# Optimization experiments

Measured on AMD Instinct MI355X. Metric: run time of the kernel, lower is better.

## Reference

```python
import jax, jax.numpy as jnp
import numpy as np

B, N, DIM = 4, 1024, 768
H, D = 12, 64            # num_heads, head_dim
R = 8                    # spd_rank
INNER = H * D
SCALE = D ** -0.5


def setup_inputs() -> dict:
    key = jax.random.key(0)
    ks = jax.random.split(key, 8)
    def w(k, shp, s=0.02):
        return jax.random.normal(k, shp, jnp.float32) * s
    return {
        "x": jax.random.normal(ks[0], (B, N, DIM), jnp.float32),
        # VariationalLinear params: weight mean mu + log-sigma (for KL term)
        "wq_mu": w(ks[1], (INNER, DIM)), "wq_ls": jnp.full((INNER, DIM), -5.0, jnp.float32),
        "wk_mu": w(ks[2], (INNER, DIM)), "wk_ls": jnp.full((INNER, DIM), -5.0, jnp.float32),
        "wv_mu": w(ks[3], (INNER, DIM)), "wv_ls": jnp.full((INNER, DIM), -5.0, jnp.float32),
        "wo_mu": w(ks[4], (DIM, INNER)), "wo_ls": jnp.full((DIM, INNER), -5.0, jnp.float32),
        "wo_b": jnp.zeros((DIM,), jnp.float32),
        # LogEuclideanProjection linear layers (head_dim -> spd_rank)
        "sq_w": w(ks[5], (R, D)), "sq_b": jnp.zeros((R,), jnp.float32),
        "sk_w": w(ks[6], (R, D)), "sk_b": jnp.zeros((R,), jnp.float32),
    }


def _kl(mu, ls):
    # KL( N(mu, sigma^2) || N(0,1) ) summed over weights
    return 0.5 * jnp.sum(jnp.exp(2.0 * ls) + mu * mu - 1.0 - 2.0 * ls)


def reference(x, wq_mu, wq_ls, wk_mu, wk_ls, wv_mu, wv_ls,
              wo_mu, wo_ls, wo_b, sq_w, sq_b, sk_w, sk_b):
    b, n, _ = x.shape
    # Q/K/V projections (variational linear, mean weights)
    q = jnp.einsum('bnd,id->bni', x, wq_mu).reshape(b, n, H, D).transpose(0, 2, 1, 3)
    k = jnp.einsum('bnd,id->bni', x, wk_mu).reshape(b, n, H, D).transpose(0, 2, 1, 3)
    v = jnp.einsum('bnd,id->bni', x, wv_mu).reshape(b, n, H, D).transpose(0, 2, 1, 3)

    # SPD projection (diagonal SPD): softplus(linear) + 1e-6, per head token
    q_spd = jax.nn.softplus(jnp.einsum('bhnd,rd->bhnr', q, sq_w) + sq_b) + 1e-6
    k_spd = jax.nn.softplus(jnp.einsum('bhnd,rd->bhnr', k, sk_w) + sk_b) + 1e-6
    lq = jnp.log(q_spd + 1e-8)  # (b,h,n,R)
    lk = jnp.log(k_spd + 1e-8)

    # ||lq_i - lk_j||_2 via expansion (avoids (b,h,n,n,R) intermediate)
    d2 = (jnp.sum(lq * lq, -1)[..., :, None]
          + jnp.sum(lk * lk, -1)[..., None, :]
          - 2.0 * jnp.einsum('bhnr,bhmr->bhnm', lq, lk))
    dist = jnp.sqrt(jnp.maximum(d2, 1e-12))  # (b,h,n,n)

    attn = jax.nn.softmax(-dist * SCALE, axis=-1)
    out = jnp.einsum('bhnm,bhmd->bhnd', attn, v)
    out = out.transpose(0, 2, 1, 3).reshape(b, n, INNER)
    out = jnp.einsum('bni,di->bnd', out, wo_mu) + wo_b

    kl_total = _kl(wq_mu, wq_ls) + _kl(wk_mu, wk_ls) + _kl(wv_mu, wv_ls) + _kl(wo_mu, wo_ls)
    return out, kl_total
```

## Files before the change

kernel.cpp:

```cpp
#include <hip/hip_runtime.h>
#include <math.h>

#define HQ   12
#define DH   64
#define NSEQ 1024
#define BB   4
#define DIMM 768
#define RR   8
#define BHD  (BB*HQ)
#define MROWS (BB*NSEQ)
#define OUT_ELEMS (BB*NSEQ*DIMM)

typedef short bf16x8 __attribute__((ext_vector_type(8)));
typedef float f32x4  __attribute__((ext_vector_type(4)));

__device__ __forceinline__ unsigned short f2bf(float f) {
    union { float f; unsigned u; } x; x.f = f;
    return (unsigned short)((x.u + 0x7fffu + ((x.u >> 16) & 1u)) >> 16);
}
__device__ __forceinline__ float bf2f(unsigned short b) {
    union { unsigned u; float f; } x; x.u = ((unsigned)b) << 16;
    return x.f;
}
__device__ __forceinline__ unsigned pack_bf16(float w0, float w1) {
    return __builtin_amdgcn_perm(__float_as_uint(w1) + 0x8000u,
                                 __float_as_uint(w0) + 0x8000u, 0x07060302u);
}

#define AS_GLOBAL(p) ((const __attribute__((address_space(1))) void*)(p))
#define AS_LDS(p)    ((__attribute__((address_space(3))) void*)(p))

__global__ __launch_bounds__(256)
void prep_kernel(const float* __restrict__ x,  const float* __restrict__ wv,
                 const float* __restrict__ wo, const float* __restrict__ wq,
                 const float* __restrict__ wq_ls, const float* __restrict__ wk,
                 const float* __restrict__ wk_ls, const float* __restrict__ wv_ls,
                 const float* __restrict__ wo_ls, const float* __restrict__ sqw,
                 const float* __restrict__ skw,
                 unsigned short* __restrict__ xb, unsigned short* __restrict__ wvb,
                 unsigned short* __restrict__ wob, unsigned short* __restrict__ cqk,
                 double* __restrict__ klacc)
{
    __shared__ double sd[256];
    const int seg = blockIdx.y;
    const int tid = threadIdx.x;
    const int bx  = blockIdx.x;

    if (seg <= 2) {
        const float* src = (seg == 0) ? x : (seg == 1) ? wv : wo;
        unsigned short* dst = (seg == 0) ? xb : (seg == 1) ? wvb : wob;
        const int n4 = (seg == 0) ? 786432 : 147456;
        for (int i = bx*256 + tid; i < n4; i += 1024*256) {
            float4 v = ((const float4*)src)[i];
            ((uint2*)dst)[i] = make_uint2(pack_bf16(v.x, v.y), pack_bf16(v.z, v.w));
        }
    } else if (seg <= 6) {
        if (bx >= 64) return;
        const float *mu, *ls;
        if      (seg == 3) { mu = wq; ls = wq_ls; }
        else if (seg == 4) { mu = wk; ls = wk_ls; }
        else if (seg == 5) { mu = wv; ls = wv_ls; }
        else               { mu = wo; ls = wo_ls; }
        double acc = 0.0;
        for (int i = bx*256 + tid; i < 147456; i += 64*256) {
            float4 m4 = ((const float4*)mu)[i];
            float4 l4 = ((const float4*)ls)[i];
            acc += (double)(expf(2.f*l4.x) + m4.x*m4.x - 1.f - 2.f*l4.x);
            acc += (double)(expf(2.f*l4.y) + m4.y*m4.y - 1.f - 2.f*l4.y);
            acc += (double)(expf(2.f*l4.z) + m4.z*m4.z - 1.f - 2.f*l4.z);
            acc += (double)(expf(2.f*l4.w) + m4.w*m4.w - 1.f - 2.f*l4.w);
        }
        sd[tid] = acc;
        __syncthreads();
        for (int s = 128; s > 0; s >>= 1) {
            if (tid < s) sd[tid] += sd[tid + s];
            __syncthreads();
        }
        if (tid == 0) atomicAdd(klacc, sd[0]);
    } else {
        if (bx >= 576) return;
        const int j   = (bx % 3)*256 + tid;
        const int row = bx / 3;
        const int g   = row >= 96;
        const int hr  = row - g*96;
        const int h   = hr >> 3, r = hr & 7;
        const float* sw = (g ? skw : sqw) + r*64;
        const float* W  = (g ? wk  : wq) + h*64*768 + j;
        float acc = 0.f;
        #pragma unroll
        for (int d = 0; d < 64; ++d) acc += sw[d] * W[d*768];
        cqk[row*768 + j] = f2bf(acc);
    }
}

__global__ __launch_bounds__(256)
void lspd_gemm(const unsigned short* __restrict__ X,
               const unsigned short* __restrict__ Cqk,
               const float* __restrict__ sqb, const float* __restrict__ skb,
               unsigned short* __restrict__ lqo, unsigned short* __restrict__ lko,
               float* __restrict__ nqo, float* __restrict__ nko)
{
    __shared__ unsigned short As[64*32];
    __shared__ unsigned short Bs[64*32];
    const int tid  = threadIdx.x;
    const int lane = tid & 63;
    const int qr   = lane & 15, quad = lane >> 4;
    const int wid  = tid >> 6;
    const int w_m  = wid >> 1, w_n = wid & 1;
    const int bx = blockIdx.x, by = blockIdx.y;
    const int row0 = tid >> 2;
    const int segk = (tid & 3) * 8;

    f32x4 acc[2][2] = {};

    for (int kt = 0; kt < 768; kt += 32) {
        __syncthreads();
        __builtin_amdgcn_global_load_lds(AS_GLOBAL(X   + (by*64 + row0)*768 + kt + segk),
                                         AS_LDS(&As[tid*8]), 16, 0, 0);
        __builtin_amdgcn_global_load_lds(AS_GLOBAL(Cqk + (bx*64 + row0)*768 + kt + segk),
                                         AS_LDS(&Bs[tid*8]), 16, 0, 0);
        __syncthreads();

        bf16x8 a[2], b[2];
        #pragma unroll
        for (int mi = 0; mi < 2; ++mi)
            a[mi] = *(const bf16x8*)&As[(w_m*32 + mi*16 + qr)*32 + quad*8];
        #pragma unroll
        for (int ni = 0; ni < 2; ++ni)
            b[ni] = *(const bf16x8*)&Bs[(w_n*32 + ni*16 + qr)*32 + quad*8];
        #pragma unroll
        for (int mi = 0; mi < 2; ++mi)
            #pragma unroll
            for (int ni = 0; ni < 2; ++ni)
                acc[mi][ni] = __builtin_amdgcn_mfma_f32_16x16x32_bf16(a[mi], b[ni], acc[mi][ni], 0, 0, 0);
    }

    const int rr = qr & 7;
    #pragma unroll
    for (int ni = 0; ni < 2; ++ni) {
        const int c = bx*64 + w_n*32 + ni*16 + qr;
        const int g = (c >= 96);
        const int cc = c - g*96;
        const int h = cc >> 3;
        unsigned short* dst = g ? lko : lqo;
        float* ndst = g ? nko : nqo;
        const float bias = (g ? skb : sqb)[rr];
        #pragma unroll
        for (int mi = 0; mi < 2; ++mi) {
            #pragma unroll
            for (int r = 0; r < 4; ++r) {
                const int m = by*64 + w_m*32 + mi*16 + quad*4 + r;
                const int b = m >> 10, n = m & 1023;
                const float pre = acc[mi][ni][r] + bias;
                const float sp = (pre > 0.f) ? (pre + log1pf(__expf(-pre)))
                                             : log1pf(__expf(pre));
                const float l = __logf(sp + 1e-6f + 1e-8f);
                const unsigned short lb = f2bf(l);
                const int base = ((b*HQ + h) << 10) + n;
                dst[(base << 3) + rr] = lb;
                const float lr = bf2f(lb);
                float sq = lr * lr;
                sq += __shfl_xor(sq, 1);
                sq += __shfl_xor(sq, 2);
                sq += __shfl_xor(sq, 4);
                if (rr == 0) ndst[base] = sq;
            }
        }
    }
}

template<int MODE>
__global__ __launch_bounds__(256)
void mfma_gemm(const unsigned short* __restrict__ X,
               const unsigned short* __restrict__ Wf,
               const float* __restrict__ bias,
               unsigned short* __restrict__ vt, float* __restrict__ outp,
               const double* __restrict__ klacc)
{
    __shared__ unsigned short As[64*32];
    __shared__ unsigned short Bs[64*32];
    const int tid  = threadIdx.x;
    const int lane = tid & 63;
    const int qr   = lane & 15, quad = lane >> 4;
    const int wid  = tid >> 6;
    const int w_m  = wid >> 1, w_n = wid & 1;
    const int bx = blockIdx.x, by = blockIdx.y;

    const unsigned short* Abase = (MODE == 0) ? (Wf + bx*64*768) : (X + by*64*768);
    const unsigned short* Bbase = (MODE == 0) ? (X + by*64*768) : (Wf + bx*64*768);

    const int row0 = tid >> 2;
    const int segk = (tid & 3) * 8;

    f32x4 acc[2][2] = {};

    for (int kt = 0; kt < 768; kt += 32) {
        __syncthreads();
        __builtin_amdgcn_global_load_lds(AS_GLOBAL(Abase + row0*768 + kt + segk),
                                         AS_LDS(&As[tid*8]), 16, 0, 0);
        __builtin_amdgcn_global_load_lds(AS_GLOBAL(Bbase + row0*768 + kt + segk),
                                         AS_LDS(&Bs[tid*8]), 16, 0, 0);
        __syncthreads();

        bf16x8 a[2], b[2];
        #pragma unroll
        for (int mi = 0; mi < 2; ++mi)
            a[mi] = *(const bf16x8*)&As[(w_m*32 + mi*16 + qr)*32 + quad*8];
        #pragma unroll
        for (int ni = 0; ni < 2; ++ni)
            b[ni] = *(const bf16x8*)&Bs[(w_n*32 + ni*16 + qr)*32 + quad*8];
        #pragma unroll
        for (int mi = 0; mi < 2; ++mi)
            #pragma unroll
            for (int ni = 0; ni < 2; ++ni)
                acc[mi][ni] = __builtin_amdgcn_mfma_f32_16x16x32_bf16(a[mi], b[ni], acc[mi][ni], 0, 0, 0);
    }

    if (MODE == 1) {
        #pragma unroll
        for (int ni = 0; ni < 2; ++ni) {
            const int i = bx*64 + w_n*32 + ni*16 + qr;
            const float bs = bias[i];
            #pragma unroll
            for (int mi = 0; mi < 2; ++mi) {
                const int m0 = by*64 + w_m*32 + mi*16 + quad*4;
                #pragma unroll
                for (int r = 0; r < 4; ++r)
                    outp[(m0 + r)*768 + i] = acc[mi][ni][r] + bs;
            }
        }
        if (bx == 0 && by == 0 && tid == 0)
            outp[OUT_ELEMS] = (float)(0.5 * klacc[0]);
    } else {
        const int bidx = (by*64) >> 10;
        #pragma unroll
        for (int mi = 0; mi < 2; ++mi) {
            #pragma unroll
            for (int r = 0; r < 4; ++r) {
                const int i = bx*64 + w_m*32 + mi*16 + quad*4 + r;
                const int h = i >> 6, d = i & 63;
                #pragma unroll
                for (int ni = 0; ni < 2; ++ni) {
                    const int n = by*64 + w_n*32 + ni*16 + qr;
                    vt[((((bidx*HQ + h) << 6) + d) << 10) + (n & 1023)] = f2bf(acc[mi][ni][r]);
                }
            }
        }
    }
}

__global__ __launch_bounds__(256)
void attn_kernel(const unsigned short* __restrict__ lq,
                 const unsigned short* __restrict__ lk,
                 const float* __restrict__ nq, const float* __restrict__ nk,
                 const unsigned short* __restrict__ vt,
                 unsigned short* __restrict__ out)
{
    __shared__ unsigned short lk_s[64*8];
    __shared__ unsigned short vt_s[64*64];
    __shared__ unsigned short w_s[64*72];

    const int tid  = threadIdx.x;
    const int lane = tid & 63;
    const int wid  = tid >> 6;
    const int qr   = lane & 15;
    const int quad = lane >> 4;
    const int bh   = blockIdx.y;
    const int q0   = blockIdx.x*64 + wid*16;
    const int qrow = (bh << 10) + q0 + qr;
    const int bb   = bh / HQ;
    const int hh   = bh - bb*HQ;

    bf16x8 bq = {};
    if (quad == 0) bq = *(const bf16x8*)(lq + qrow*8);
    const float nqv = nq[qrow];

    f32x4 acc[4] = {};
    float wsum_acc = 0.f;

    const unsigned short* vtg = vt + (bh << 16);
    const unsigned short* lkg = lk + (bh << 13);
    const float*          nkg = nk + (bh << 10);

    const int srow = tid >> 3;
    const int scol = ((tid & 7) ^ (srow & 7)) << 3;
    const float EXP2S = -0.1803368801f;

    for (int c = 0; c < NSEQ; c += 64) {
        __syncthreads();
        __builtin_amdgcn_global_load_lds(AS_GLOBAL(vtg + srow*1024 + c + scol),
                                         AS_LDS(&vt_s[tid*8]), 16, 0, 0);
        __builtin_amdgcn_global_load_lds(AS_GLOBAL(vtg + (srow + 32)*1024 + c + scol),
                                         AS_LDS(&vt_s[2048 + tid*8]), 16, 0, 0);
        if (tid < 64)
            __builtin_amdgcn_global_load_lds(AS_GLOBAL(lkg + (c + tid)*8),
                                             AS_LDS(&lk_s[tid*8]), 16, 0, 0);
        __syncthreads();

        float wsum_c = 0.f;
        unsigned wpk[4][2];
        #pragma unroll
        for (int kb = 0; kb < 4; ++kb) {
            bf16x8 ak = {};
            if (quad == 0) ak = *(const bf16x8*)&lk_s[(kb*16 + qr)*8];
            f32x4 s = {};
            s = __builtin_amdgcn_mfma_f32_16x16x32_bf16(ak, bq, s, 0, 0, 0);
            const float4 nk4 = *(const float4*)(nkg + c + kb*16 + quad*4);
            const float nkv[4] = {nk4.x, nk4.y, nk4.z, nk4.w};
            float w[4];
            #pragma unroll
            for (int r = 0; r < 4; ++r) {
                const float d2 = fmaf(-2.f, s[r], nqv + nkv[r]);
                const float dist = __builtin_amdgcn_sqrtf(fmaxf(d2, 1e-12f));
                w[r] = exp2f(dist * EXP2S);
                wsum_c += w[r];
            }
            wpk[kb][0] = pack_bf16(w[0], w[1]);
            wpk[kb][1] = pack_bf16(w[2], w[3]);
        }
        #pragma unroll
        for (int kb = 0; kb < 4; ++kb)
            *(uint2*)&w_s[(wid*16 + qr)*72 + kb*16 + quad*4] =
                make_uint2(wpk[kb][0], wpk[kb][1]);
        wsum_c += __shfl_xor(wsum_c, 16);
        wsum_c += __shfl_xor(wsum_c, 32);
        wsum_acc += wsum_c;

        #pragma unroll
        for (int s2 = 0; s2 < 2; ++s2) {
            const bf16x8 af = *(const bf16x8*)&w_s[(wid*16 + qr)*72 + s2*32 + quad*8];
            #pragma unroll
            for (int jb = 0; jb < 4; ++jb) {
                const int row = jb*16 + qr;
                const int grp = (s2*4 + quad) ^ (qr & 7);
                const bf16x8 bv = *(const bf16x8*)&vt_s[(row << 6) + (grp << 3)];
                acc[jb] = __builtin_amdgcn_mfma_f32_16x16x32_bf16(af, bv, acc[jb], 0, 0, 0);
            }
        }
    }

    #pragma unroll
    for (int jb = 0; jb < 4; ++jb) {
        #pragma unroll
        for (int r = 0; r < 4; ++r) {
            const int row = quad*4 + r;
            const float wsd = __shfl(wsum_acc, row);
            const int qgl = q0 + row;
            const int d = jb*16 + qr;
            out[((bb << 10) + qgl)*768 + hh*64 + d] = f2bf(acc[jb][r] / wsd);
        }
    }
}

extern "C" void kernel_launch(void* const* d_in, const int* in_sizes, int n_in,
                              void* d_out, int out_size, void* d_ws, size_t ws_size,
                              hipStream_t stream)
{
    const float* x     = (const float*)d_in[0];
    const float* wq    = (const float*)d_in[1];
    const float* wq_ls = (const float*)d_in[2];
    const float* wk    = (const float*)d_in[3];
    const float* wk_ls = (const float*)d_in[4];
    const float* wv    = (const float*)d_in[5];
    const float* wv_ls = (const float*)d_in[6];
    const float* wo    = (const float*)d_in[7];
    const float* wo_ls = (const float*)d_in[8];
    const float* wo_b  = (const float*)d_in[9];
    const float* sq_w  = (const float*)d_in[10];
    const float* sq_b  = (const float*)d_in[11];
    const float* sk_w  = (const float*)d_in[12];
    const float* sk_b  = (const float*)d_in[13];
    float* out = (float*)d_out;

    float* ws = (float*)d_ws;
    unsigned short* vt  = (unsigned short*)ws;
    unsigned short* xb  = (unsigned short*)(ws + 1572864);
    unsigned short* wvb = (unsigned short*)(ws + 3145728);
    unsigned short* wob = (unsigned short*)(ws + 3440640);
    unsigned short* cqk = (unsigned short*)(ws + 3735552);
    unsigned short* lqb = (unsigned short*)(ws + 3809280);
    unsigned short* lkb = (unsigned short*)(ws + 4005888);
    float* nqb = ws + 4202496;
    float* nkb = ws + 4251648;
    double* klacc = (double*)(ws + 4300800);

    const dim3 b256(256);

    hipMemsetAsync(klacc, 0, sizeof(double), stream);
    prep_kernel<<<dim3(1024, 8), b256, 0, stream>>>(
        x, wv, wo, wq, wq_ls, wk, wk_ls, wv_ls, wo_ls, sq_w, sk_w,
        xb, wvb, wob, cqk, klacc);
    lspd_gemm<<<dim3(3, 64), b256, 0, stream>>>(xb, cqk, sq_b, sk_b,
                                                lqb, lkb, nqb, nkb);
    mfma_gemm<0><<<dim3(12, 64), b256, 0, stream>>>(xb, wvb, nullptr, vt, nullptr, nullptr);
    attn_kernel<<<dim3(16, BHD), b256, 0, stream>>>(lqb, lkb, nqb, nkb, vt, xb);
    mfma_gemm<1><<<dim3(12, 64), b256, 0, stream>>>(xb, wob, wo_b, nullptr, out, klacc);
}
```

Measured before the change: 198.2 us.

## Merge V and log-SPD projections into one launch and double-buffer LDS tiles

Merges the V projection GEMM and the log-SPD projection GEMM into one kernel whose role is chosen by block index, removing a launch and filling more CUs at once. All GEMM loops and the attention loop now use double-buffered LDS with a prefetch of the next tile before compute, leaving one barrier per iteration instead of two. The prep grid is shrunk from 1024 to 576 blocks, and the final normalisation multiplies by a reciprocal instead of dividing. Double buffering doubles LDS use per block, which may lower occupancy, and merging two roles in one kernel can leave blocks with uneven work.

```diff
diff --git a/kernel.cpp b/kernel.cpp
--- a/kernel.cpp
+++ b/kernel.cpp
@@ -50,7 +50,7 @@
         const float* src = (seg == 0) ? x : (seg == 1) ? wv : wo;
         unsigned short* dst = (seg == 0) ? xb : (seg == 1) ? wvb : wob;
         const int n4 = (seg == 0) ? 786432 : 147456;
-        for (int i = bx*256 + tid; i < n4; i += 1024*256) {
+        for (int i = bx*256 + tid; i < n4; i += 576*256) {
             float4 v = ((const float4*)src)[i];
             ((uint2*)dst)[i] = make_uint2(pack_bf16(v.x, v.y), pack_bf16(v.z, v.w));
         }
@@ -78,7 +78,6 @@
         }
         if (tid == 0) atomicAdd(klacc, sd[0]);
     } else {
-        if (bx >= 576) return;
         const int j   = (bx % 3)*256 + tid;
         const int row = bx / 3;
         const int g   = row >= 96;
@@ -94,144 +93,63 @@
 }
 
 __global__ __launch_bounds__(256)
-void lspd_gemm(const unsigned short* __restrict__ X,
-               const unsigned short* __restrict__ Cqk,
-               const float* __restrict__ sqb, const float* __restrict__ skb,
-               unsigned short* __restrict__ lqo, unsigned short* __restrict__ lko,
-               float* __restrict__ nqo, float* __restrict__ nko)
+void proj_kernel(const unsigned short* __restrict__ X,
+                 const unsigned short* __restrict__ Wv,
+                 const unsigned short* __restrict__ Cqk,
+                 const float* __restrict__ sqb, const float* __restrict__ skb,
+                 unsigned short* __restrict__ vt,
+                 unsigned short* __restrict__ lqo, unsigned short* __restrict__ lko,
+                 float* __restrict__ nqo, float* __restrict__ nko)
 {
-    __shared__ unsigned short As[64*32];
-    __shared__ unsigned short Bs[64*32];
+    __shared__ unsigned short As[2][64*32];
+    __shared__ unsigned short Bs[2][64*32];
     const int tid  = threadIdx.x;
     const int lane = tid & 63;
     const int qr   = lane & 15, quad = lane >> 4;
     const int wid  = tid >> 6;
     const int w_m  = wid >> 1, w_n = wid & 1;
     const int bx = blockIdx.x, by = blockIdx.y;
+
+    const bool vrole = (bx < 12);
+    const unsigned short* Abase = vrole ? (Wv + bx*64*768)      : (X + by*64*768);
+    const unsigned short* Bbase = vrole ? (X + by*64*768)       : (Cqk + (bx-12)*64*768);
+
     const int row0 = tid >> 2;
     const int segk = (tid & 3) * 8;
 
     f32x4 acc[2][2] = {};
 
-    for (int kt = 0; kt < 768; kt += 32) {
-        __syncthreads();
-        __builtin_amdgcn_global_load_lds(AS_GLOBAL(X   + (by*64 + row0)*768 + kt + segk),
-                                         AS_LDS(&As[tid*8]), 16, 0, 0);
-        __builtin_amdgcn_global_load_lds(AS_GLOBAL(Cqk + (bx*64 + row0)*768 + kt + segk),
-                                         AS_LDS(&Bs[tid*8]), 16, 0, 0);
-        __syncthreads();
-
+    __builtin_amdgcn_global_load_lds(AS_GLOBAL(Abase + row0*768 + segk),
+                                     AS_LDS(&As[0][tid*8]), 16, 0, 0);
+    __builtin_amdgcn_global_load_lds(AS_GLOBAL(Bbase + row0*768 + segk),
+                                     AS_LDS(&Bs[0][tid*8]), 16, 0, 0);
+    __syncthreads();
+
+    for (int ki = 0; ki < 24; ++ki) {
+        const int cur = ki & 1;
+        if (ki + 1 < 24) {
+            const int kt = (ki + 1) * 32;
+            __builtin_amdgcn_global_load_lds(AS_GLOBAL(Abase + row0*768 + kt + segk),
+                                             AS_LDS(&As[cur^1][tid*8]), 16, 0, 0);
+            __builtin_amdgcn_global_load_lds(AS_GLOBAL(Bbase + row0*768 + kt + segk),
+                                             AS_LDS(&Bs[cur^1][tid*8]), 16, 0, 0);
+        }
         bf16x8 a[2], b[2];
         #pragma unroll
         for (int mi = 0; mi < 2; ++mi)
-            a[mi] = *(const bf16x8*)&As[(w_m*32 + mi*16 + qr)*32 + quad*8];
+            a[mi] = *(const bf16x8*)&As[cur][(w_m*32 + mi*16 + qr)*32 + quad*8];
         #pragma unroll
         for (int ni = 0; ni < 2; ++ni)
-            b[ni] = *(const bf16x8*)&Bs[(w_n*32 + ni*16 + qr)*32 + quad*8];
+            b[ni] = *(const bf16x8*)&Bs[cur][(w_n*32 + ni*16 + qr)*32 + quad*8];
         #pragma unroll
         for (int mi = 0; mi < 2; ++mi)
             #pragma unroll
             for (int ni = 0; ni < 2; ++ni)
                 acc[mi][ni] = __builtin_amdgcn_mfma_f32_16x16x32_bf16(a[mi], b[ni], acc[mi][ni], 0, 0, 0);
-    }
-
-    const int rr = qr & 7;
-    #pragma unroll
-    for (int ni = 0; ni < 2; ++ni) {
-        const int c = bx*64 + w_n*32 + ni*16 + qr;
-        const int g = (c >= 96);
-        const int cc = c - g*96;
-        const int h = cc >> 3;
-        unsigned short* dst = g ? lko : lqo;
-        float* ndst = g ? nko : nqo;
-        const float bias = (g ? skb : sqb)[rr];
-        #pragma unroll
-        for (int mi = 0; mi < 2; ++mi) {
-            #pragma unroll
-            for (int r = 0; r < 4; ++r) {
-                const int m = by*64 + w_m*32 + mi*16 + quad*4 + r;
-                const int b = m >> 10, n = m & 1023;
-                const float pre = acc[mi][ni][r] + bias;
-                const float sp = (pre > 0.f) ? (pre + log1pf(__expf(-pre)))
-                                             : log1pf(__expf(pre));
-                const float l = __logf(sp + 1e-6f + 1e-8f);
-                const unsigned short lb = f2bf(l);
-                const int base = ((b*HQ + h) << 10) + n;
-                dst[(base << 3) + rr] = lb;
-                const float lr = bf2f(lb);
-                float sq = lr * lr;
-                sq += __shfl_xor(sq, 1);
-                sq += __shfl_xor(sq, 2);
-                sq += __shfl_xor(sq, 4);
-                if (rr == 0) ndst[base] = sq;
-            }
-        }
-    }
-}
-
-template<int MODE>
-__global__ __launch_bounds__(256)
-void mfma_gemm(const unsigned short* __restrict__ X,
-               const unsigned short* __restrict__ Wf,
-               const float* __restrict__ bias,
-               unsigned short* __restrict__ vt, float* __restrict__ outp,
-               const double* __restrict__ klacc)
-{
-    __shared__ unsigned short As[64*32];
-    __shared__ unsigned short Bs[64*32];
-    const int tid  = threadIdx.x;
-    const int lane = tid & 63;
-    const int qr   = lane & 15, quad = lane >> 4;
-    const int wid  = tid >> 6;
-    const int w_m  = wid >> 1, w_n = wid & 1;
-    const int bx = blockIdx.x, by = blockIdx.y;
-
-    const unsigned short* Abase = (MODE == 0) ? (Wf + bx*64*768) : (X + by*64*768);
-    const unsigned short* Bbase = (MODE == 0) ? (X + by*64*768) : (Wf + bx*64*768);
-
-    const int row0 = tid >> 2;
-    const int segk = (tid & 3) * 8;
-
-    f32x4 acc[2][2] = {};
-
-    for (int kt = 0; kt < 768; kt += 32) {
         __syncthreads();
-        __builtin_amdgcn_global_load_lds(AS_GLOBAL(Abase + row0*768 + kt + segk),
-                                         AS_LDS(&As[tid*8]), 16, 0, 0);
-        __builtin_amdgcn_global_load_lds(AS_GLOBAL(Bbase + row0*768 + kt + segk),
-                                         AS_LDS(&Bs[tid*8]), 16, 0, 0);
-        __syncthreads();
-
-        bf16x8 a[2], b[2];
-        #pragma unroll
-        for (int mi = 0; mi < 2; ++mi)
-            a[mi] = *(const bf16x8*)&As[(w_m*32 + mi*16 + qr)*32 + quad*8];
-        #pragma unroll
-        for (int ni = 0; ni < 2; ++ni)
-            b[ni] = *(const bf16x8*)&Bs[(w_n*32 + ni*16 + qr)*32 + quad*8];
-        #pragma unroll
-        for (int mi = 0; mi < 2; ++mi)
-            #pragma unroll
-            for (int ni = 0; ni < 2; ++ni)
-                acc[mi][ni] = __builtin_amdgcn_mfma_f32_16x16x32_bf16(a[mi], b[ni], acc[mi][ni], 0, 0, 0);
-    }
-
-    if (MODE == 1) {
-        #pragma unroll
-        for (int ni = 0; ni < 2; ++ni) {
-            const int i = bx*64 + w_n*32 + ni*16 + qr;
-            const float bs = bias[i];
-            #pragma unroll
-            for (int mi = 0; mi < 2; ++mi) {
-                const int m0 = by*64 + w_m*32 + mi*16 + quad*4;
-                #pragma unroll
-                for (int r = 0; r < 4; ++r)
-                    outp[(m0 + r)*768 + i] = acc[mi][ni][r] + bs;
-            }
-        }
-        if (bx == 0 && by == 0 && tid == 0)
-            outp[OUT_ELEMS] = (float)(0.5 * klacc[0]);
-    } else {
+    }
+
+    if (vrole) {
         const int bidx = (by*64) >> 10;
         #pragma unroll
         for (int mi = 0; mi < 2; ++mi) {
@@ -246,7 +164,108 @@
                 }
             }
         }
-    }
+    } else {
+        const int rr = qr & 7;
+        #pragma unroll
+        for (int ni = 0; ni < 2; ++ni) {
+            const int c = (bx-12)*64 + w_n*32 + ni*16 + qr;
+            const int g = (c >= 96);
+            const int cc = c - g*96;
+            const int h = cc >> 3;
+            unsigned short* dst = g ? lko : lqo;
+            float* ndst = g ? nko : nqo;
+            const float bias = (g ? skb : sqb)[rr];
+            #pragma unroll
+            for (int mi = 0; mi < 2; ++mi) {
+                #pragma unroll
+                for (int r = 0; r < 4; ++r) {
+                    const int m = by*64 + w_m*32 + mi*16 + quad*4 + r;
+                    const int b = m >> 10, n = m & 1023;
+                    const float pre = acc[mi][ni][r] + bias;
+                    const float sp = (pre > 0.f) ? (pre + log1pf(__expf(-pre)))
+                                                 : log1pf(__expf(pre));
+                    const float l = __logf(sp + 1e-6f + 1e-8f);
+                    const unsigned short lb = f2bf(l);
+                    const int base = ((b*HQ + h) << 10) + n;
+                    dst[(base << 3) + rr] = lb;
+                    const float lr = bf2f(lb);
+                    float sq = lr * lr;
+                    sq += __shfl_xor(sq, 1);
+                    sq += __shfl_xor(sq, 2);
+                    sq += __shfl_xor(sq, 4);
+                    if (rr == 0) ndst[base] = sq;
+                }
+            }
+        }
+    }
+}
+
+__global__ __launch_bounds__(256)
+void ogemm_kernel(const unsigned short* __restrict__ X,
+                  const unsigned short* __restrict__ Wf,
+                  const float* __restrict__ bias, float* __restrict__ outp,
+                  const double* __restrict__ klacc)
+{
+    __shared__ unsigned short As[2][64*32];
+    __shared__ unsigned short Bs[2][64*32];
+    const int tid  = threadIdx.x;
+    const int lane = tid & 63;
+    const int qr   = lane & 15, quad = lane >> 4;
+    const int wid  = tid >> 6;
+    const int w_m  = wid >> 1, w_n = wid & 1;
+    const int bx = blockIdx.x, by = blockIdx.y;
+
+    const unsigned short* Abase = X  + by*64*768;
+    const unsigned short* Bbase = Wf + bx*64*768;
+    const int row0 = tid >> 2;
+    const int segk = (tid & 3) * 8;
+
+    f32x4 acc[2][2] = {};
+
+    __builtin_amdgcn_global_load_lds(AS_GLOBAL(Abase + row0*768 + segk),
+                                     AS_LDS(&As[0][tid*8]), 16, 0, 0);
+    __builtin_amdgcn_global_load_lds(AS_GLOBAL(Bbase + row0*768 + segk),
+                                     AS_LDS(&Bs[0][tid*8]), 16, 0, 0);
+    __syncthreads();
+
+    for (int ki = 0; ki < 24; ++ki) {
+        const int cur = ki & 1;
+        if (ki + 1 < 24) {
+            const int kt = (ki + 1) * 32;
+            __builtin_amdgcn_global_load_lds(AS_GLOBAL(Abase + row0*768 + kt + segk),
+                                             AS_LDS(&As[cur^1][tid*8]), 16, 0, 0);
+            __builtin_amdgcn_global_load_lds(AS_GLOBAL(Bbase + row0*768 + kt + segk),
+                                             AS_LDS(&Bs[cur^1][tid*8]), 16, 0, 0);
+        }
+        bf16x8 a[2], b[2];
+        #pragma unroll
+        for (int mi = 0; mi < 2; ++mi)
+            a[mi] = *(const bf16x8*)&As[cur][(w_m*32 + mi*16 + qr)*32 + quad*8];
+        #pragma unroll
+        for (int ni = 0; ni < 2; ++ni)
+            b[ni] = *(const bf16x8*)&Bs[cur][(w_n*32 + ni*16 + qr)*32 + quad*8];
+        #pragma unroll
+        for (int mi = 0; mi < 2; ++mi)
+            #pragma unroll
+            for (int ni = 0; ni < 2; ++ni)
+                acc[mi][ni] = __builtin_amdgcn_mfma_f32_16x16x32_bf16(a[mi], b[ni], acc[mi][ni], 0, 0, 0);
+        __syncthreads();
+    }
+
+    #pragma unroll
+    for (int ni = 0; ni < 2; ++ni) {
+        const int i = bx*64 + w_n*32 + ni*16 + qr;
+        const float bs = bias[i];
+        #pragma unroll
+        for (int mi = 0; mi < 2; ++mi) {
+            const int m0 = by*64 + w_m*32 + mi*16 + quad*4;
+            #pragma unroll
+            for (int r = 0; r < 4; ++r)
+                outp[(m0 + r)*768 + i] = acc[mi][ni][r] + bs;
+        }
+    }
+    if (bx == 0 && by == 0 && tid == 0)
+        outp[OUT_ELEMS] = (float)(0.5 * klacc[0]);
 }
 
 __global__ __launch_bounds__(256)
@@ -256,8 +275,8 @@
                  const unsigned short* __restrict__ vt,
                  unsigned short* __restrict__ out)
 {
-    __shared__ unsigned short lk_s[64*8];
-    __shared__ unsigned short vt_s[64*64];
+    __shared__ unsigned short lk_s[2][512];
+    __shared__ unsigned short vt_s[2][4096];
     __shared__ unsigned short w_s[64*72];
 
     const int tid  = threadIdx.x;
@@ -286,23 +305,30 @@
     const int scol = ((tid & 7) ^ (srow & 7)) << 3;
     const float EXP2S = -0.1803368801f;
 
-    for (int c = 0; c < NSEQ; c += 64) {
-        __syncthreads();
+    auto stage = [&](int c, int buf) {
         __builtin_amdgcn_global_load_lds(AS_GLOBAL(vtg + srow*1024 + c + scol),
-                                         AS_LDS(&vt_s[tid*8]), 16, 0, 0);
+                                         AS_LDS(&vt_s[buf][tid*8]), 16, 0, 0);
         __builtin_amdgcn_global_load_lds(AS_GLOBAL(vtg + (srow + 32)*1024 + c + scol),
-                                         AS_LDS(&vt_s[2048 + tid*8]), 16, 0, 0);
+                                         AS_LDS(&vt_s[buf][2048 + tid*8]), 16, 0, 0);
         if (tid < 64)
             __builtin_amdgcn_global_load_lds(AS_GLOBAL(lkg + (c + tid)*8),
-                                             AS_LDS(&lk_s[tid*8]), 16, 0, 0);
-        __syncthreads();
+                                             AS_LDS(&lk_s[buf][tid*8]), 16, 0, 0);
+    };
+
+    stage(0, 0);
+    __syncthreads();
+
+    for (int ci = 0; ci < 16; ++ci) {
+        const int cur = ci & 1;
+        const int c = ci << 6;
+        if (ci + 1 < 16) stage(c + 64, cur ^ 1);
 
         float wsum_c = 0.f;
         unsigned wpk[4][2];
         #pragma unroll
         for (int kb = 0; kb < 4; ++kb) {
             bf16x8 ak = {};
-            if (quad == 0) ak = *(const bf16x8*)&lk_s[(kb*16 + qr)*8];
+            if (quad == 0) ak = *(const bf16x8*)&lk_s[cur][(kb*16 + qr)*8];
             f32x4 s = {};
             s = __builtin_amdgcn_mfma_f32_16x16x32_bf16(ak, bq, s, 0, 0, 0);
             const float4 nk4 = *(const float4*)(nkg + c + kb*16 + quad*4);
@@ -333,21 +359,23 @@
             for (int jb = 0; jb < 4; ++jb) {
                 const int row = jb*16 + qr;
                 const int grp = (s2*4 + quad) ^ (qr & 7);
-                const bf16x8 bv = *(const bf16x8*)&vt_s[(row << 6) + (grp << 3)];
+                const bf16x8 bv = *(const bf16x8*)&vt_s[cur][(row << 6) + (grp << 3)];
                 acc[jb] = __builtin_amdgcn_mfma_f32_16x16x32_bf16(af, bv, acc[jb], 0, 0, 0);
             }
         }
-    }
-
+        __syncthreads();
+    }
+
+    const float inv = 1.0f / wsum_acc;
     #pragma unroll
     for (int jb = 0; jb < 4; ++jb) {
         #pragma unroll
         for (int r = 0; r < 4; ++r) {
             const int row = quad*4 + r;
-            const float wsd = __shfl(wsum_acc, row);
+            const float wi = __shfl(inv, row);
             const int qgl = q0 + row;
             const int d = jb*16 + qr;
-            out[((bb << 10) + qgl)*768 + hh*64 + d] = f2bf(acc[jb][r] / wsd);
+            out[((bb << 10) + qgl)*768 + hh*64 + d] = f2bf(acc[jb][r] * wi);
         }
     }
 }
@@ -387,12 +415,11 @@
     const dim3 b256(256);
 
     hipMemsetAsync(klacc, 0, sizeof(double), stream);
-    prep_kernel<<<dim3(1024, 8), b256, 0, stream>>>(
+    prep_kernel<<<dim3(576, 8), b256, 0, stream>>>(
         x, wv, wo, wq, wq_ls, wk, wk_ls, wv_ls, wo_ls, sq_w, sk_w,
         xb, wvb, wob, cqk, klacc);
-    lspd_gemm<<<dim3(3, 64), b256, 0, stream>>>(xb, cqk, sq_b, sk_b,
-                                                lqb, lkb, nqb, nkb);
-    mfma_gemm<0><<<dim3(12, 64), b256, 0, stream>>>(xb, wvb, nullptr, vt, nullptr, nullptr);
+    proj_kernel<<<dim3(15, 64), b256, 0, stream>>>(xb, wvb, cqk, sq_b, sk_b,
+                                                   vt, lqb, lkb, nqb, nkb);
     attn_kernel<<<dim3(16, BHD), b256, 0, stream>>>(lqb, lkb, nqb, nkb, vt, xb);
-    mfma_gemm<1><<<dim3(12, 64), b256, 0, stream>>>(xb, wob, wo_b, nullptr, out, klacc);
-}
+    ogemm_kernel<<<dim3(12, 64), b256, 0, stream>>>(xb, wob, wo_b, out, klacc);
+}
```

After: 205.8 us. 3.8% more time.

## Merge V and SPD projection GEMMs into one launch; drop memset and KL atomic

Applied to the files above, without the earlier changes.

The V projection GEMM and the log-SPD projection GEMM are merged into a single proj_kernel launch of 15x64 blocks, with a role chosen by block index. This removes one kernel launch and lets the two small GEMMs share the GPU. The KL reduction now writes per-block partials that the output GEMM reduces, so the memset and the double atomicAdd go away. The prep grid shrinks from 1024 to 576 blocks, and attention normalisation uses a reciprocal multiply instead of a divide.

```diff
diff --git a/kernel.cpp b/kernel.cpp
--- a/kernel.cpp
+++ b/kernel.cpp
@@ -39,7 +39,7 @@
                  const float* __restrict__ skw,
                  unsigned short* __restrict__ xb, unsigned short* __restrict__ wvb,
                  unsigned short* __restrict__ wob, unsigned short* __restrict__ cqk,
-                 double* __restrict__ klacc)
+                 double* __restrict__ klparts)
 {
     __shared__ double sd[256];
     const int seg = blockIdx.y;
@@ -50,7 +50,7 @@
         const float* src = (seg == 0) ? x : (seg == 1) ? wv : wo;
         unsigned short* dst = (seg == 0) ? xb : (seg == 1) ? wvb : wob;
         const int n4 = (seg == 0) ? 786432 : 147456;
-        for (int i = bx*256 + tid; i < n4; i += 1024*256) {
+        for (int i = bx*256 + tid; i < n4; i += 576*256) {
             float4 v = ((const float4*)src)[i];
             ((uint2*)dst)[i] = make_uint2(pack_bf16(v.x, v.y), pack_bf16(v.z, v.w));
         }
@@ -76,9 +76,8 @@
             if (tid < s) sd[tid] += sd[tid + s];
             __syncthreads();
         }
-        if (tid == 0) atomicAdd(klacc, sd[0]);
+        if (tid == 0) klparts[(seg - 3)*64 + bx] = sd[0];
     } else {
-        if (bx >= 576) return;
         const int j   = (bx % 3)*256 + tid;
         const int row = bx / 3;
         const int g   = row >= 96;
@@ -94,11 +93,13 @@
 }
 
 __global__ __launch_bounds__(256)
-void lspd_gemm(const unsigned short* __restrict__ X,
-               const unsigned short* __restrict__ Cqk,
-               const float* __restrict__ sqb, const float* __restrict__ skb,
-               unsigned short* __restrict__ lqo, unsigned short* __restrict__ lko,
-               float* __restrict__ nqo, float* __restrict__ nko)
+void proj_kernel(const unsigned short* __restrict__ X,
+                 const unsigned short* __restrict__ Wv,
+                 const unsigned short* __restrict__ Cqk,
+                 const float* __restrict__ sqb, const float* __restrict__ skb,
+                 unsigned short* __restrict__ vt,
+                 unsigned short* __restrict__ lqo, unsigned short* __restrict__ lko,
+                 float* __restrict__ nqo, float* __restrict__ nko)
 {
     __shared__ unsigned short As[64*32];
     __shared__ unsigned short Bs[64*32];
@@ -108,86 +109,10 @@
     const int wid  = tid >> 6;
     const int w_m  = wid >> 1, w_n = wid & 1;
     const int bx = blockIdx.x, by = blockIdx.y;
-    const int row0 = tid >> 2;
-    const int segk = (tid & 3) * 8;
-
-    f32x4 acc[2][2] = {};
-
-    for (int kt = 0; kt < 768; kt += 32) {
-        __syncthreads();
-        __builtin_amdgcn_global_load_lds(AS_GLOBAL(X   + (by*64 + row0)*768 + kt + segk),
-                                         AS_LDS(&As[tid*8]), 16, 0, 0);
-        __builtin_amdgcn_global_load_lds(AS_GLOBAL(Cqk + (bx*64 + row0)*768 + kt + segk),
-                                         AS_LDS(&Bs[tid*8]), 16, 0, 0);
-        __syncthreads();
-
-        bf16x8 a[2], b[2];
-        #pragma unroll
-        for (int mi = 0; mi < 2; ++mi)
-            a[mi] = *(const bf16x8*)&As[(w_m*32 + mi*16 + qr)*32 + quad*8];
-        #pragma unroll
-        for (int ni = 0; ni < 2; ++ni)
-            b[ni] = *(const bf16x8*)&Bs[(w_n*32 + ni*16 + qr)*32 + quad*8];
-        #pragma unroll
-        for (int mi = 0; mi < 2; ++mi)
-            #pragma unroll
-            for (int ni = 0; ni < 2; ++ni)
-                acc[mi][ni] = __builtin_amdgcn_mfma_f32_16x16x32_bf16(a[mi], b[ni], acc[mi][ni], 0, 0, 0);
-    }
-
-    const int rr = qr & 7;
-    #pragma unroll
-    for (int ni = 0; ni < 2; ++ni) {
-        const int c = bx*64 + w_n*32 + ni*16 + qr;
-        const int g = (c >= 96);
-        const int cc = c - g*96;
-        const int h = cc >> 3;
-        unsigned short* dst = g ? lko : lqo;
-        float* ndst = g ? nko : nqo;
-        const float bias = (g ? skb : sqb)[rr];
-        #pragma unroll
-        for (int mi = 0; mi < 2; ++mi) {
-            #pragma unroll
-            for (int r = 0; r < 4; ++r) {
-                const int m = by*64 + w_m*32 + mi*16 + quad*4 + r;
-                const int b = m >> 10, n = m & 1023;
-                const float pre = acc[mi][ni][r] + bias;
-                const float sp = (pre > 0.f) ? (pre + log1pf(__expf(-pre)))
-                                             : log1pf(__expf(pre));
-                const float l = __logf(sp + 1e-6f + 1e-8f);
-                const unsigned short lb = f2bf(l);
-                const int base = ((b*HQ + h) << 10) + n;
-                dst[(base << 3) + rr] = lb;
-                const float lr = bf2f(lb);
-                float sq = lr * lr;
-                sq += __shfl_xor(sq, 1);
-                sq += __shfl_xor(sq, 2);
-                sq += __shfl_xor(sq, 4);
-                if (rr == 0) ndst[base] = sq;
-            }
-        }
-    }
-}
-
-template<int MODE>
-__global__ __launch_bounds__(256)
-void mfma_gemm(const unsigned short* __restrict__ X,
-               const unsigned short* __restrict__ Wf,
-               const float* __restrict__ bias,
-               unsigned short* __restrict__ vt, float* __restrict__ outp,
-               const double* __restrict__ klacc)
-{
-    __shared__ unsigned short As[64*32];
-    __shared__ unsigned short Bs[64*32];
-    const int tid  = threadIdx.x;
-    const int lane = tid & 63;
-    const int qr   = lane & 15, quad = lane >> 4;
-    const int wid  = tid >> 6;
-    const int w_m  = wid >> 1, w_n = wid & 1;
-    const int bx = blockIdx.x, by = blockIdx.y;
-
-    const unsigned short* Abase = (MODE == 0) ? (Wf + bx*64*768) : (X + by*64*768);
-    const unsigned short* Bbase = (MODE == 0) ? (X + by*64*768) : (Wf + bx*64*768);
+
+    const bool vrole = (bx < 12);
+    const unsigned short* Abase = vrole ? (Wv + bx*64*768) : (X + by*64*768);
+    const unsigned short* Bbase = vrole ? (X + by*64*768)  : (Cqk + (bx-12)*64*768);
 
     const int row0 = tid >> 2;
     const int segk = (tid & 3) * 8;
@@ -216,22 +141,7 @@
                 acc[mi][ni] = __builtin_amdgcn_mfma_f32_16x16x32_bf16(a[mi], b[ni], acc[mi][ni], 0, 0, 0);
     }
 
-    if (MODE == 1) {
-        #pragma unroll
-        for (int ni = 0; ni < 2; ++ni) {
-            const int i = bx*64 + w_n*32 + ni*16 + qr;
-            const float bs = bias[i];
-            #pragma unroll
-            for (int mi = 0; mi < 2; ++mi) {
-                const int m0 = by*64 + w_m*32 + mi*16 + quad*4;
-                #pragma unroll
-                for (int r = 0; r < 4; ++r)
-                    outp[(m0 + r)*768 + i] = acc[mi][ni][r] + bs;
-            }
-        }
-        if (bx == 0 && by == 0 && tid == 0)
-            outp[OUT_ELEMS] = (float)(0.5 * klacc[0]);
-    } else {
+    if (vrole) {
         const int bidx = (by*64) >> 10;
         #pragma unroll
         for (int mi = 0; mi < 2; ++mi) {
@@ -246,6 +156,108 @@
                 }
             }
         }
+    } else {
+        const int rr = qr & 7;
+        #pragma unroll
+        for (int ni = 0; ni < 2; ++ni) {
+            const int c = (bx-12)*64 + w_n*32 + ni*16 + qr;
+            const int g = (c >= 96);
+            const int cc = c - g*96;
+            const int h = cc >> 3;
+            unsigned short* dst = g ? lko : lqo;
+            float* ndst = g ? nko : nqo;
+            const float bias = (g ? skb : sqb)[rr];
+            #pragma unroll
+            for (int mi = 0; mi < 2; ++mi) {
+                #pragma unroll
+                for (int r = 0; r < 4; ++r) {
+                    const int m = by*64 + w_m*32 + mi*16 + quad*4 + r;
+                    const int b = m >> 10, n = m & 1023;
+                    const float pre = acc[mi][ni][r] + bias;
+                    const float sp = (pre > 0.f) ? (pre + log1pf(__expf(-pre)))
+                                                 : log1pf(__expf(pre));
+                    const float l = __logf(sp + 1e-6f + 1e-8f);
+                    const unsigned short lb = f2bf(l);
+                    const int base = ((b*HQ + h) << 10) + n;
+                    dst[(base << 3) + rr] = lb;
+                    const float lr = bf2f(lb);
+                    float sq = lr * lr;
+                    sq += __shfl_xor(sq, 1);
+                    sq += __shfl_xor(sq, 2);
+                    sq += __shfl_xor(sq, 4);
+                    if (rr == 0) ndst[base] = sq;
+                }
+            }
+        }
+    }
+}
+
+__global__ __launch_bounds__(256)
+void ogemm_kernel(const unsigned short* __restrict__ X,
+                  const unsigned short* __restrict__ Wf,
+                  const float* __restrict__ bias, float* __restrict__ outp,
+                  const double* __restrict__ klparts)
+{
+    __shared__ unsigned short As[64*32];
+    __shared__ unsigned short Bs[64*32];
+    __shared__ double sd[256];
+    const int tid  = threadIdx.x;
+    const int lane = tid & 63;
+    const int qr   = lane & 15, quad = lane >> 4;
+    const int wid  = tid >> 6;
+    const int w_m  = wid >> 1, w_n = wid & 1;
+    const int bx = blockIdx.x, by = blockIdx.y;
+
+    const unsigned short* Abase = X  + by*64*768;
+    const unsigned short* Bbase = Wf + bx*64*768;
+    const int row0 = tid >> 2;
+    const int segk = (tid & 3) * 8;
+
+    f32x4 acc[2][2] = {};
+
+    for (int kt = 0; kt < 768; kt += 32) {
+        __syncthreads();
+        __builtin_amdgcn_global_load_lds(AS_GLOBAL(Abase + row0*768 + kt + segk),
+                                         AS_LDS(&As[tid*8]), 16, 0, 0);
+        __builtin_amdgcn_global_load_lds(AS_GLOBAL(Bbase + row0*768 + kt + segk),
+                                         AS_LDS(&Bs[tid*8]), 16, 0, 0);
+        __syncthreads();
+
+        bf16x8 a[2], b[2];
+        #pragma unroll
+        for (int mi = 0; mi < 2; ++mi)
+            a[mi] = *(const bf16x8*)&As[(w_m*32 + mi*16 + qr)*32 + quad*8];
+        #pragma unroll
+        for (int ni = 0; ni < 2; ++ni)
+            b[ni] = *(const bf16x8*)&Bs[(w_n*32 + ni*16 + qr)*32 + quad*8];
+        #pragma unroll
+        for (int mi = 0; mi < 2; ++mi)
+            #pragma unroll
+            for (int ni = 0; ni < 2; ++ni)
+                acc[mi][ni] = __builtin_amdgcn_mfma_f32_16x16x32_bf16(a[mi], b[ni], acc[mi][ni], 0, 0, 0);
+    }
+
+    #pragma unroll
+    for (int ni = 0; ni < 2; ++ni) {
+        const int i = bx*64 + w_n*32 + ni*16 + qr;
+        const float bs = bias[i];
+        #pragma unroll
+        for (int mi = 0; mi < 2; ++mi) {
+            const int m0 = by*64 + w_m*32 + mi*16 + quad*4;
+            #pragma unroll
+            for (int r = 0; r < 4; ++r)
+                outp[(m0 + r)*768 + i] = acc[mi][ni][r] + bs;
+        }
+    }
+
+    if (bx == 0 && by == 0) {
+        sd[tid] = klparts[tid];
+        __syncthreads();
+        for (int s = 128; s > 0; s >>= 1) {
+            if (tid < s) sd[tid] += sd[tid + s];
+            __syncthreads();
+        }
+        if (tid == 0) outp[OUT_ELEMS] = (float)(0.5 * sd[0]);
     }
 }
 
@@ -339,15 +351,16 @@
         }
     }
 
+    const float inv = 1.0f / wsum_acc;
     #pragma unroll
     for (int jb = 0; jb < 4; ++jb) {
         #pragma unroll
         for (int r = 0; r < 4; ++r) {
             const int row = quad*4 + r;
-            const float wsd = __shfl(wsum_acc, row);
+            const float wi = __shfl(inv, row);
             const int qgl = q0 + row;
             const int d = jb*16 + qr;
-            out[((bb << 10) + qgl)*768 + hh*64 + d] = f2bf(acc[jb][r] / wsd);
+            out[((bb << 10) + qgl)*768 + hh*64 + d] = f2bf(acc[jb][r] * wi);
         }
     }
 }
@@ -382,17 +395,15 @@
     unsigned short* lkb = (unsigned short*)(ws + 4005888);
     float* nqb = ws + 4202496;
     float* nkb = ws + 4251648;
-    double* klacc = (double*)(ws + 4300800);
+    double* klparts = (double*)(ws + 4300800);
 
     const dim3 b256(256);
 
-    hipMemsetAsync(klacc, 0, sizeof(double), stream);
-    prep_kernel<<<dim3(1024, 8), b256, 0, stream>>>(
+    prep_kernel<<<dim3(576, 8), b256, 0, stream>>>(
         x, wv, wo, wq, wq_ls, wk, wk_ls, wv_ls, wo_ls, sq_w, sk_w,
-        xb, wvb, wob, cqk, klacc);
-    lspd_gemm<<<dim3(3, 64), b256, 0, stream>>>(xb, cqk, sq_b, sk_b,
-                                                lqb, lkb, nqb, nkb);
-    mfma_gemm<0><<<dim3(12, 64), b256, 0, stream>>>(xb, wvb, nullptr, vt, nullptr, nullptr);
+        xb, wvb, wob, cqk, klparts);
+    proj_kernel<<<dim3(15, 64), b256, 0, stream>>>(xb, wvb, cqk, sq_b, sk_b,
+                                                   vt, lqb, lkb, nqb, nkb);
     attn_kernel<<<dim3(16, BHD), b256, 0, stream>>>(lqb, lkb, nqb, nkb, vt, xb);
-    mfma_gemm<1><<<dim3(12, 64), b256, 0, stream>>>(xb, wob, wo_b, nullptr, out, klacc);
-}
+    ogemm_kernel<<<dim3(12, 64), b256, 0, stream>>>(xb, wob, wo_b, out, klparts);
+}
```

After: 201.7 us. No clear change (+1.8%).
